# Optimization experiments

Hardware: AMD Instinct MI355X
Metric: run time of the kernel (lower is better)

Reference implementation:

```python
import jax, jax.numpy as jnp
import numpy as np

INPUT_DIM = 512
HIDDEN_DIM = 512
T, B = 512, 128


def setup_inputs() -> dict:
    key = jax.random.key(0)
    ks = jax.random.split(key, 9)
    s_in = 1.0 / np.sqrt(INPUT_DIM + HIDDEN_DIM)
    d = INPUT_DIM + HIDDEN_DIM
    inputs = jax.random.normal(ks[0], (T, B, INPUT_DIM), dtype=jnp.float32)
    def lin(kw, kb):
        W = jax.random.uniform(kw, (HIDDEN_DIM, d), minval=-s_in, maxval=s_in, dtype=jnp.float32)
        b = jax.random.uniform(kb, (HIDDEN_DIM,), minval=-s_in, maxval=s_in, dtype=jnp.float32)
        return W, b
    Wf, bf = lin(ks[1], ks[2])
    Wi, bi = lin(ks[3], ks[4])
    Wg, bg = lin(ks[5], ks[6])
    Wo, bo = lin(ks[7], ks[8])
    return {"inputs": inputs, "Wf": Wf, "bf": bf, "Wi": Wi, "bi": bi,
            "Wg": Wg, "bg": bg, "Wo": Wo, "bo": bo}


def _lstm(inputs, Wf, bf, Wi, bi, Wg, bg, Wo, bo):
    B_ = inputs.shape[1]
    h0 = jnp.zeros((B_, HIDDEN_DIM), dtype=inputs.dtype)
    c0 = jnp.zeros((B_, HIDDEN_DIM), dtype=inputs.dtype)

    def step(carry, x):
        hx, cx = carry
        combined = jnp.concatenate([x, hx], axis=1)  # [B, input+hidden]
        f = jax.nn.sigmoid(combined @ Wf.T + bf)
        i = jax.nn.sigmoid(combined @ Wi.T + bi)
        g = jnp.tanh(combined @ Wg.T + bg)
        o = jax.nn.sigmoid(combined @ Wo.T + bo)
        cx = f * cx + i * g
        hx = o * jnp.tanh(cx)
        return (hx, cx), hx

    (hx, cx), outputs = jax.lax.scan(step, (h0, c0), inputs)
    return outputs, (hx, cx)


def reference(inputs, Wf, bf, Wi, bi, Wg, bg, Wo, bo):
    return _lstm(inputs, Wf, bf, Wi, bi, Wg, bg, Wo, bo)
```

## Files before the change

kernel.cpp:

```cpp
#include <hip/hip_runtime.h>
#include <stdint.h>

#define T_STEPS 512
#define BATCH   128
#define HID     512
#define KTOT    1024

typedef __attribute__((ext_vector_type(8))) short          bf16x8;
typedef __attribute__((ext_vector_type(8))) unsigned short u16x8;
typedef __attribute__((ext_vector_type(4))) float          f32x4;

__device__ inline unsigned short f2bf(float f) {
    union { float f; unsigned u; } x; x.f = f;
    unsigned r = x.u + 0x7FFFu + ((x.u >> 16) & 1u);
    return (unsigned short)(r >> 16);
}

__device__ inline float sigmoidf_(float x) { return 1.f / (1.f + __expf(-x)); }
__device__ inline float tanhf_(float x)    { float e = __expf(2.f * x); return 1.f - 2.f / (e + 1.f); }

__global__ void cast_x_kernel(const float* __restrict__ x, unsigned short* __restrict__ y, int n) {
    int i = (blockIdx.x * blockDim.x + threadIdx.x) * 8;
    if (i >= n) return;
    float4 a = *(const float4*)(x + i);
    float4 b = *(const float4*)(x + i + 4);
    u16x8 v;
    v[0] = f2bf(a.x); v[1] = f2bf(a.y); v[2] = f2bf(a.z); v[3] = f2bf(a.w);
    v[4] = f2bf(b.x); v[5] = f2bf(b.y); v[6] = f2bf(b.z); v[7] = f2bf(b.w);
    *(u16x8*)(y + i) = v;
}

__device__ inline void load_x32(const float* xf, const unsigned short* xbf, int use_xbf,
                                size_t off, uint4& a, uint4& b) {
    if (use_xbf) {
        const uint4* p = (const uint4*)(xbf + off);
        a = p[0]; b = p[1];
    } else {
        const float4* p = (const float4*)(xf + off);
        float4 f0 = p[0], f1 = p[1], f2 = p[2], f3 = p[3];
        u16x8 v;
        v[0] = f2bf(f0.x); v[1] = f2bf(f0.y); v[2] = f2bf(f0.z); v[3] = f2bf(f0.w);
        v[4] = f2bf(f1.x); v[5] = f2bf(f1.y); v[6] = f2bf(f1.z); v[7] = f2bf(f1.w);
        a = *(uint4*)&v;
        u16x8 w;
        w[0] = f2bf(f2.x); w[1] = f2bf(f2.y); w[2] = f2bf(f2.z); w[3] = f2bf(f2.w);
        w[4] = f2bf(f3.x); w[5] = f2bf(f3.y); w[6] = f2bf(f3.z); w[7] = f2bf(f3.w);
        b = *(uint4*)&w;
    }
}

__global__ __launch_bounds__(512, 2) void lstm_kernel(
    const float* __restrict__ xf,
    const unsigned short* __restrict__ xbf,
    const float* __restrict__ Wf, const float* __restrict__ bfv,
    const float* __restrict__ Wi, const float* __restrict__ biv,
    const float* __restrict__ Wg, const float* __restrict__ bgv,
    const float* __restrict__ Wo, const float* __restrict__ bov,
    float* __restrict__ out,
    unsigned int* __restrict__ flags,
    unsigned short* __restrict__ hbuf,
    int use_xbf)
{
    __shared__ __align__(16) unsigned short comb[16][1048];
    __shared__ float gatesl[4][16][33];

    const int tid  = threadIdx.x;
    const int bgc  = blockIdx.x >> 4;
    const int cg   = blockIdx.x & 15;
    const int w    = tid >> 6;
    const int lane = tid & 63;
    const int gate = w & 3;
    const int uh   = w >> 2;
    const int n    = lane & 15;
    const int quad = lane >> 4;
    const int unit = cg * 32 + uh * 16 + n;

    const float* Wp = (gate == 0) ? Wf : (gate == 1) ? Wi : (gate == 2) ? Wg : Wo;
    const float* bp = (gate == 0) ? bfv : (gate == 1) ? biv : (gate == 2) ? bgv : bov;
    const float bias = bp[unit];

    bf16x8 wfr[32];
    const float* wrow = Wp + (size_t)unit * KTOT;
#pragma unroll
    for (int kk = 0; kk < 32; ++kk) {
        const float4* p = (const float4*)(wrow + kk * 32 + quad * 8);
        float4 a = p[0], b = p[1];
        u16x8 v;
        v[0] = f2bf(a.x); v[1] = f2bf(a.y); v[2] = f2bf(a.z); v[3] = f2bf(a.w);
        v[4] = f2bf(b.x); v[5] = f2bf(b.y); v[6] = f2bf(b.z); v[7] = f2bf(b.w);
        wfr[kk] = (bf16x8)v;
    }

    const int srow = tid >> 5;
    const int scol = tid & 31;

    const int bc = srow, uc = scol;
    float creg = 0.f;
    const int bglob = bgc * 16 + bc;
    const int uglob = cg * 32 + uc;

    const size_t xstride = (size_t)HID;

    {
        uint4 a, b;
        load_x32(xf, xbf, use_xbf, ((size_t)(0 * BATCH + bgc * 16 + srow)) * xstride + scol * 16, a, b);
        *(uint4*)&comb[srow][scol * 16]     = a;
        *(uint4*)&comb[srow][scol * 16 + 8] = b;
        uint4 z = {0u, 0u, 0u, 0u};
        *(uint4*)&comb[srow][512 + scol * 16]     = z;
        *(uint4*)&comb[srow][512 + scol * 16 + 8] = z;
    }
    __syncthreads();

    f32x4 axa = {0.f, 0.f, 0.f, 0.f}, axb = {0.f, 0.f, 0.f, 0.f};
#pragma unroll
    for (int kk = 0; kk < 16; kk += 2) {
        bf16x8 a0 = *(const bf16x8*)&comb[n][kk * 32 + quad * 8];
        bf16x8 a1 = *(const bf16x8*)&comb[n][(kk + 1) * 32 + quad * 8];
        axa = __builtin_amdgcn_mfma_f32_16x16x32_bf16(a0, wfr[kk],     axa, 0, 0, 0);
        axb = __builtin_amdgcn_mfma_f32_16x16x32_bf16(a1, wfr[kk + 1], axb, 0, 0, 0);
    }

    uint4 pfa, pfb;
    load_x32(xf, xbf, use_xbf, ((size_t)(1 * BATCH + bgc * 16 + srow)) * xstride + scol * 16, pfa, pfb);

    for (int t = 0; t < T_STEPS; ++t) {
        if (t > 0) {
            if (lane < 16) {
                unsigned int* fp = flags + ((size_t)(t - 1) * 8 + bgc) * 16 + lane;
                while (__hip_atomic_load(fp, __ATOMIC_RELAXED, __HIP_MEMORY_SCOPE_AGENT) == 0u) {}
            }
            const unsigned long long* src = (const unsigned long long*)
                (hbuf + (size_t)((t - 1) & 1) * BATCH * HID + (size_t)(bgc * 16 + srow) * HID + scol * 16);
            unsigned long long v0 = __hip_atomic_load(src + 0, __ATOMIC_RELAXED, __HIP_MEMORY_SCOPE_AGENT);
            unsigned long long v1 = __hip_atomic_load(src + 1, __ATOMIC_RELAXED, __HIP_MEMORY_SCOPE_AGENT);
            unsigned long long v2 = __hip_atomic_load(src + 2, __ATOMIC_RELAXED, __HIP_MEMORY_SCOPE_AGENT);
            unsigned long long v3 = __hip_atomic_load(src + 3, __ATOMIC_RELAXED, __HIP_MEMORY_SCOPE_AGENT);
            uint4 a, b;
            a.x = (unsigned)v0; a.y = (unsigned)(v0 >> 32);
            a.z = (unsigned)v1; a.w = (unsigned)(v1 >> 32);
            b.x = (unsigned)v2; b.y = (unsigned)(v2 >> 32);
            b.z = (unsigned)v3; b.w = (unsigned)(v3 >> 32);
            *(uint4*)&comb[srow][512 + scol * 16]     = a;
            *(uint4*)&comb[srow][512 + scol * 16 + 8] = b;
        }
        __syncthreads();

#pragma unroll
        for (int kk = 16; kk < 32; kk += 2) {
            bf16x8 a0 = *(const bf16x8*)&comb[n][kk * 32 + quad * 8];
            bf16x8 a1 = *(const bf16x8*)&comb[n][(kk + 1) * 32 + quad * 8];
            axa = __builtin_amdgcn_mfma_f32_16x16x32_bf16(a0, wfr[kk],     axa, 0, 0, 0);
            axb = __builtin_amdgcn_mfma_f32_16x16x32_bf16(a1, wfr[kk + 1], axb, 0, 0, 0);
        }

#pragma unroll
        for (int r = 0; r < 4; ++r) {
            float v = axa[r] + axb[r] + bias;
            v = (gate == 2) ? tanhf_(v) : sigmoidf_(v);
            gatesl[gate][quad * 4 + r][uh * 16 + n] = v;
        }
        if (t + 1 < T_STEPS) {
            *(uint4*)&comb[srow][scol * 16]     = pfa;
            *(uint4*)&comb[srow][scol * 16 + 8] = pfb;
        }
        __syncthreads();

        {
            float fv = gatesl[0][bc][uc], iv = gatesl[1][bc][uc];
            float gv = gatesl[2][bc][uc], ov = gatesl[3][bc][uc];
            float cn = fv * creg + iv * gv;
            creg = cn;
            float hv = ov * tanhf_(cn);
            unsigned int us  = (unsigned int)f2bf(hv);
            unsigned int us1 = (unsigned int)__shfl_down((int)us, 1);
            if ((uc & 1) == 0) {
                unsigned int pv = us | (us1 << 16);
                unsigned int* hp = (unsigned int*)(hbuf + (size_t)(t & 1) * BATCH * HID
                                                   + (size_t)bglob * HID + uglob);
                __hip_atomic_store(hp, pv, __ATOMIC_RELAXED, __HIP_MEMORY_SCOPE_AGENT);
            }
            out[(size_t)t * BATCH * HID + (size_t)bglob * HID + uglob] = hv;
            if (t == T_STEPS - 1) {
                out[(size_t)T_STEPS * BATCH * HID + (size_t)bglob * HID + uglob] = hv;
                out[(size_t)T_STEPS * BATCH * HID + BATCH * HID + (size_t)bglob * HID + uglob] = cn;
            }
        }

        if (t + 1 < T_STEPS) {
            axa = (f32x4){0.f, 0.f, 0.f, 0.f};
            axb = (f32x4){0.f, 0.f, 0.f, 0.f};
#pragma unroll
            for (int kk = 0; kk < 16; kk += 2) {
                bf16x8 a0 = *(const bf16x8*)&comb[n][kk * 32 + quad * 8];
                bf16x8 a1 = *(const bf16x8*)&comb[n][(kk + 1) * 32 + quad * 8];
                axa = __builtin_amdgcn_mfma_f32_16x16x32_bf16(a0, wfr[kk],     axa, 0, 0, 0);
                axb = __builtin_amdgcn_mfma_f32_16x16x32_bf16(a1, wfr[kk + 1], axb, 0, 0, 0);
            }
        }

        __builtin_amdgcn_s_waitcnt(0);
        __syncthreads();
        if (tid == 0) {
            __hip_atomic_store(flags + ((size_t)t * 8 + bgc) * 16 + cg, 1u,
                               __ATOMIC_RELAXED, __HIP_MEMORY_SCOPE_AGENT);
        }
        if (t + 2 < T_STEPS) {
            load_x32(xf, xbf, use_xbf,
                     ((size_t)((t + 2) * BATCH + bgc * 16 + srow)) * xstride + scol * 16, pfa, pfb);
        }
    }
}

extern "C" void kernel_launch(void* const* d_in, const int* in_sizes, int n_in,
                              void* d_out, int out_size, void* d_ws, size_t ws_size,
                              hipStream_t stream) {
    (void)in_sizes; (void)n_in; (void)out_size;
    const float* x   = (const float*)d_in[0];
    const float* Wf  = (const float*)d_in[1];
    const float* bfv = (const float*)d_in[2];
    const float* Wi  = (const float*)d_in[3];
    const float* biv = (const float*)d_in[4];
    const float* Wg  = (const float*)d_in[5];
    const float* bgv = (const float*)d_in[6];
    const float* Wo  = (const float*)d_in[7];
    const float* bov = (const float*)d_in[8];
    float* out = (float*)d_out;

    unsigned char* ws = (unsigned char*)d_ws;
    unsigned int*   flags = (unsigned int*)ws;
    unsigned short* hbuf  = (unsigned short*)(ws + 262144);
    unsigned short* xbf   = (unsigned short*)(ws + 524288);

    size_t need = 524288 + (size_t)T_STEPS * BATCH * HID * 2;
    int use_xbf = (ws_size >= need) ? 1 : 0;

    hipMemsetAsync(flags, 0, 262144, stream);
    if (use_xbf) {
        int nelem = T_STEPS * BATCH * HID;
        cast_x_kernel<<<nelem / (256 * 8), 256, 0, stream>>>(x, xbf, nelem);
    }
    lstm_kernel<<<dim3(128), dim3(512), 0, stream>>>(
        x, xbf, Wf, bfv, Wi, biv, Wg, bgv, Wo, bov, out, flags, hbuf, use_xbf);
}
```

Baseline: 1.940 ms.

## Replace per-step flag barrier with step-tagged h packets polled directly

Removes the separate flag array and the per-step waitcnt plus block barrier plus flag store. Each hidden-state word pair is now written as a 64-bit packet that carries the step number, so consumers poll the data itself until every tag matches. The next step's h is loaded speculatively at the end of each iteration to hide latency. The trade-off is that the h exchange traffic doubles and each thread spins on eight loads instead of a few lanes spinning on one flag.

New measurement: 2.226 ms. 1.15x slower.

```diff
diff --git a/kernel.cpp b/kernel.cpp
--- a/kernel.cpp
+++ b/kernel.cpp
@@ -5,6 +5,7 @@
 #define BATCH   128
 #define HID     512
 #define KTOT    1024
+#define HPAIRS  (BATCH * 256)
 
 typedef __attribute__((ext_vector_type(8))) short          bf16x8;
 typedef __attribute__((ext_vector_type(8))) unsigned short u16x8;
@@ -57,8 +58,7 @@
     const float* __restrict__ Wg, const float* __restrict__ bgv,
     const float* __restrict__ Wo, const float* __restrict__ bov,
     float* __restrict__ out,
-    unsigned int* __restrict__ flags,
-    unsigned short* __restrict__ hbuf,
+    unsigned long long* __restrict__ hbuf,
     int use_xbf)
 {
     __shared__ __align__(16) unsigned short comb[16][1048];
@@ -98,12 +98,13 @@
     float creg = 0.f;
     const int bglob = bgc * 16 + bc;
     const int uglob = cg * 32 + uc;
+    const int bgrow = bgc * 16 + srow;
 
     const size_t xstride = (size_t)HID;
 
     {
         uint4 a, b;
-        load_x32(xf, xbf, use_xbf, ((size_t)(0 * BATCH + bgc * 16 + srow)) * xstride + scol * 16, a, b);
+        load_x32(xf, xbf, use_xbf, ((size_t)(0 * BATCH + bgrow)) * xstride + scol * 16, a, b);
         *(uint4*)&comb[srow][scol * 16]     = a;
         *(uint4*)&comb[srow][scol * 16 + 8] = b;
         uint4 z = {0u, 0u, 0u, 0u};
@@ -122,25 +123,31 @@
     }
 
     uint4 pfa, pfb;
-    load_x32(xf, xbf, use_xbf, ((size_t)(1 * BATCH + bgc * 16 + srow)) * xstride + scol * 16, pfa, pfb);
+    load_x32(xf, xbf, use_xbf, ((size_t)(1 * BATCH + bgrow)) * xstride + scol * 16, pfa, pfb);
+
+    unsigned long long pv[8];
 
     for (int t = 0; t < T_STEPS; ++t) {
         if (t > 0) {
-            if (lane < 16) {
-                unsigned int* fp = flags + ((size_t)(t - 1) * 8 + bgc) * 16 + lane;
-                while (__hip_atomic_load(fp, __ATOMIC_RELAXED, __HIP_MEMORY_SCOPE_AGENT) == 0u) {}
-            }
-            const unsigned long long* src = (const unsigned long long*)
-                (hbuf + (size_t)((t - 1) & 1) * BATCH * HID + (size_t)(bgc * 16 + srow) * HID + scol * 16);
-            unsigned long long v0 = __hip_atomic_load(src + 0, __ATOMIC_RELAXED, __HIP_MEMORY_SCOPE_AGENT);
-            unsigned long long v1 = __hip_atomic_load(src + 1, __ATOMIC_RELAXED, __HIP_MEMORY_SCOPE_AGENT);
-            unsigned long long v2 = __hip_atomic_load(src + 2, __ATOMIC_RELAXED, __HIP_MEMORY_SCOPE_AGENT);
-            unsigned long long v3 = __hip_atomic_load(src + 3, __ATOMIC_RELAXED, __HIP_MEMORY_SCOPE_AGENT);
+            const unsigned long long* hs = hbuf + (size_t)((t - 1) & 1) * HPAIRS
+                                         + (size_t)bgrow * 256 + (size_t)scol * 8;
+            const unsigned int want = (unsigned int)t;
+            bool ok = true;
+#pragma unroll
+            for (int j = 0; j < 8; ++j) ok = ok && ((unsigned int)(pv[j] >> 32) == want);
+            while (!ok) {
+#pragma unroll
+                for (int j = 0; j < 8; ++j)
+                    pv[j] = __hip_atomic_load(hs + j, __ATOMIC_RELAXED, __HIP_MEMORY_SCOPE_AGENT);
+                ok = true;
+#pragma unroll
+                for (int j = 0; j < 8; ++j) ok = ok && ((unsigned int)(pv[j] >> 32) == want);
+            }
             uint4 a, b;
-            a.x = (unsigned)v0; a.y = (unsigned)(v0 >> 32);
-            a.z = (unsigned)v1; a.w = (unsigned)(v1 >> 32);
-            b.x = (unsigned)v2; b.y = (unsigned)(v2 >> 32);
-            b.z = (unsigned)v3; b.w = (unsigned)(v3 >> 32);
+            a.x = (unsigned int)pv[0]; a.y = (unsigned int)pv[1];
+            a.z = (unsigned int)pv[2]; a.w = (unsigned int)pv[3];
+            b.x = (unsigned int)pv[4]; b.y = (unsigned int)pv[5];
+            b.z = (unsigned int)pv[6]; b.w = (unsigned int)pv[7];
             *(uint4*)&comb[srow][512 + scol * 16]     = a;
             *(uint4*)&comb[srow][512 + scol * 16 + 8] = b;
         }
@@ -174,11 +181,12 @@
             float hv = ov * tanhf_(cn);
             unsigned int us  = (unsigned int)f2bf(hv);
             unsigned int us1 = (unsigned int)__shfl_down((int)us, 1);
-            if ((uc & 1) == 0) {
-                unsigned int pv = us | (us1 << 16);
-                unsigned int* hp = (unsigned int*)(hbuf + (size_t)(t & 1) * BATCH * HID
-                                                   + (size_t)bglob * HID + uglob);
-                __hip_atomic_store(hp, pv, __ATOMIC_RELAXED, __HIP_MEMORY_SCOPE_AGENT);
+            if (t + 1 < T_STEPS && (uc & 1) == 0) {
+                unsigned long long pkt = ((unsigned long long)(unsigned int)(t + 1) << 32)
+                                       | (unsigned long long)(us | (us1 << 16));
+                unsigned long long* hp = hbuf + (size_t)(t & 1) * HPAIRS
+                                       + (size_t)bglob * 256 + (size_t)(uglob >> 1);
+                __hip_atomic_store(hp, pkt, __ATOMIC_RELAXED, __HIP_MEMORY_SCOPE_AGENT);
             }
             out[(size_t)t * BATCH * HID + (size_t)bglob * HID + uglob] = hv;
             if (t == T_STEPS - 1) {
@@ -199,15 +207,16 @@
             }
         }
 
-        __builtin_amdgcn_s_waitcnt(0);
-        __syncthreads();
-        if (tid == 0) {
-            __hip_atomic_store(flags + ((size_t)t * 8 + bgc) * 16 + cg, 1u,
-                               __ATOMIC_RELAXED, __HIP_MEMORY_SCOPE_AGENT);
-        }
         if (t + 2 < T_STEPS) {
             load_x32(xf, xbf, use_xbf,
-                     ((size_t)((t + 2) * BATCH + bgc * 16 + srow)) * xstride + scol * 16, pfa, pfb);
+                     ((size_t)((t + 2) * BATCH + bgrow)) * xstride + scol * 16, pfa, pfb);
+        }
+        if (t + 1 < T_STEPS) {
+            const unsigned long long* hs2 = hbuf + (size_t)(t & 1) * HPAIRS
+                                          + (size_t)bgrow * 256 + (size_t)scol * 8;
+#pragma unroll
+            for (int j = 0; j < 8; ++j)
+                pv[j] = __hip_atomic_load(hs2 + j, __ATOMIC_RELAXED, __HIP_MEMORY_SCOPE_AGENT);
         }
     }
 }
@@ -228,18 +237,17 @@
     float* out = (float*)d_out;
 
     unsigned char* ws = (unsigned char*)d_ws;
-    unsigned int*   flags = (unsigned int*)ws;
-    unsigned short* hbuf  = (unsigned short*)(ws + 262144);
-    unsigned short* xbf   = (unsigned short*)(ws + 524288);
+    unsigned long long* hbuf = (unsigned long long*)ws;
+    unsigned short*     xbf  = (unsigned short*)(ws + 524288);
 
     size_t need = 524288 + (size_t)T_STEPS * BATCH * HID * 2;
     int use_xbf = (ws_size >= need) ? 1 : 0;
 
-    hipMemsetAsync(flags, 0, 262144, stream);
+    hipMemsetAsync(hbuf, 0, 524288, stream);
     if (use_xbf) {
         int nelem = T_STEPS * BATCH * HID;
         cast_x_kernel<<<nelem / (256 * 8), 256, 0, stream>>>(x, xbf, nelem);
     }
     lstm_kernel<<<dim3(128), dim3(512), 0, stream>>>(
-        x, xbf, Wf, bfv, Wi, biv, Wg, bgv, Wo, bov, out, flags, hbuf, use_xbf);
-}
+        x, xbf, Wf, bfv, Wi, biv, Wg, bgv, Wo, bov, out, hbuf, use_xbf);
+}
```

## Replace per-block flags and barrier with per-wave atomic counter signaling

Applied to the files above, without the earlier changes.

Drops the __syncthreads before the cross-block flag store: every wave now increments one shared counter per batch group and step, and waiting waves spin on a single counter until it reaches 128 (16 blocks x 8 waves) instead of polling 16 separate flags. The output stores are moved after the signal so global writes of h no longer delay the handoff, and the last step skips the unneeded hbuf write and signal. This is meant to cut barrier and flag-polling latency on the serial critical path. The cost is contended atomic adds on one address, and correctness now relies on each wave's own waitcnt ordering its hbuf stores before its increment.

After: 3.036 ms. 1.57x slower.

```diff
diff --git a/kernel.cpp b/kernel.cpp
--- a/kernel.cpp
+++ b/kernel.cpp
@@ -57,7 +57,7 @@
     const float* __restrict__ Wg, const float* __restrict__ bgv,
     const float* __restrict__ Wo, const float* __restrict__ bov,
     float* __restrict__ out,
-    unsigned int* __restrict__ flags,
+    unsigned int* __restrict__ ctr,
     unsigned short* __restrict__ hbuf,
     int use_xbf)
 {
@@ -98,12 +98,13 @@
     float creg = 0.f;
     const int bglob = bgc * 16 + bc;
     const int uglob = cg * 32 + uc;
+    const int bgrow = bgc * 16 + srow;
 
     const size_t xstride = (size_t)HID;
 
     {
         uint4 a, b;
-        load_x32(xf, xbf, use_xbf, ((size_t)(0 * BATCH + bgc * 16 + srow)) * xstride + scol * 16, a, b);
+        load_x32(xf, xbf, use_xbf, ((size_t)(0 * BATCH + bgrow)) * xstride + scol * 16, a, b);
         *(uint4*)&comb[srow][scol * 16]     = a;
         *(uint4*)&comb[srow][scol * 16 + 8] = b;
         uint4 z = {0u, 0u, 0u, 0u};
@@ -122,16 +123,16 @@
     }
 
     uint4 pfa, pfb;
-    load_x32(xf, xbf, use_xbf, ((size_t)(1 * BATCH + bgc * 16 + srow)) * xstride + scol * 16, pfa, pfb);
+    load_x32(xf, xbf, use_xbf, ((size_t)(1 * BATCH + bgrow)) * xstride + scol * 16, pfa, pfb);
 
     for (int t = 0; t < T_STEPS; ++t) {
         if (t > 0) {
-            if (lane < 16) {
-                unsigned int* fp = flags + ((size_t)(t - 1) * 8 + bgc) * 16 + lane;
-                while (__hip_atomic_load(fp, __ATOMIC_RELAXED, __HIP_MEMORY_SCOPE_AGENT) == 0u) {}
+            if (lane == 0) {
+                const unsigned int* cp = ctr + ((size_t)(t - 1) * 8 + bgc) * 16;
+                while (__hip_atomic_load(cp, __ATOMIC_RELAXED, __HIP_MEMORY_SCOPE_AGENT) < 128u) {}
             }
             const unsigned long long* src = (const unsigned long long*)
-                (hbuf + (size_t)((t - 1) & 1) * BATCH * HID + (size_t)(bgc * 16 + srow) * HID + scol * 16);
+                (hbuf + (size_t)((t - 1) & 1) * BATCH * HID + (size_t)bgrow * HID + scol * 16);
             unsigned long long v0 = __hip_atomic_load(src + 0, __ATOMIC_RELAXED, __HIP_MEMORY_SCOPE_AGENT);
             unsigned long long v1 = __hip_atomic_load(src + 1, __ATOMIC_RELAXED, __HIP_MEMORY_SCOPE_AGENT);
             unsigned long long v2 = __hip_atomic_load(src + 2, __ATOMIC_RELAXED, __HIP_MEMORY_SCOPE_AGENT);
@@ -166,24 +167,20 @@
         }
         __syncthreads();
 
+        float hv, cn;
         {
             float fv = gatesl[0][bc][uc], iv = gatesl[1][bc][uc];
             float gv = gatesl[2][bc][uc], ov = gatesl[3][bc][uc];
-            float cn = fv * creg + iv * gv;
+            cn = fv * creg + iv * gv;
             creg = cn;
-            float hv = ov * tanhf_(cn);
+            hv = ov * tanhf_(cn);
             unsigned int us  = (unsigned int)f2bf(hv);
             unsigned int us1 = (unsigned int)__shfl_down((int)us, 1);
-            if ((uc & 1) == 0) {
+            if (t + 1 < T_STEPS && (uc & 1) == 0) {
                 unsigned int pv = us | (us1 << 16);
                 unsigned int* hp = (unsigned int*)(hbuf + (size_t)(t & 1) * BATCH * HID
                                                    + (size_t)bglob * HID + uglob);
                 __hip_atomic_store(hp, pv, __ATOMIC_RELAXED, __HIP_MEMORY_SCOPE_AGENT);
-            }
-            out[(size_t)t * BATCH * HID + (size_t)bglob * HID + uglob] = hv;
-            if (t == T_STEPS - 1) {
-                out[(size_t)T_STEPS * BATCH * HID + (size_t)bglob * HID + uglob] = hv;
-                out[(size_t)T_STEPS * BATCH * HID + BATCH * HID + (size_t)bglob * HID + uglob] = cn;
             }
         }
 
@@ -200,14 +197,19 @@
         }
 
         __builtin_amdgcn_s_waitcnt(0);
-        __syncthreads();
-        if (tid == 0) {
-            __hip_atomic_store(flags + ((size_t)t * 8 + bgc) * 16 + cg, 1u,
-                               __ATOMIC_RELAXED, __HIP_MEMORY_SCOPE_AGENT);
+        if (lane == 0 && t + 1 < T_STEPS) {
+            __hip_atomic_fetch_add(ctr + ((size_t)t * 8 + bgc) * 16, 1u,
+                                   __ATOMIC_RELAXED, __HIP_MEMORY_SCOPE_AGENT);
+        }
+
+        out[(size_t)t * BATCH * HID + (size_t)bglob * HID + uglob] = hv;
+        if (t == T_STEPS - 1) {
+            out[(size_t)T_STEPS * BATCH * HID + (size_t)bglob * HID + uglob] = hv;
+            out[(size_t)T_STEPS * BATCH * HID + BATCH * HID + (size_t)bglob * HID + uglob] = cn;
         }
         if (t + 2 < T_STEPS) {
             load_x32(xf, xbf, use_xbf,
-                     ((size_t)((t + 2) * BATCH + bgc * 16 + srow)) * xstride + scol * 16, pfa, pfb);
+                     ((size_t)((t + 2) * BATCH + bgrow)) * xstride + scol * 16, pfa, pfb);
         }
     }
 }
@@ -228,18 +230,18 @@
     float* out = (float*)d_out;
 
     unsigned char* ws = (unsigned char*)d_ws;
-    unsigned int*   flags = (unsigned int*)ws;
-    unsigned short* hbuf  = (unsigned short*)(ws + 262144);
-    unsigned short* xbf   = (unsigned short*)(ws + 524288);
+    unsigned int*   ctr  = (unsigned int*)ws;
+    unsigned short* hbuf = (unsigned short*)(ws + 262144);
+    unsigned short* xbf  = (unsigned short*)(ws + 524288);
 
     size_t need = 524288 + (size_t)T_STEPS * BATCH * HID * 2;
     int use_xbf = (ws_size >= need) ? 1 : 0;
 
-    hipMemsetAsync(flags, 0, 262144, stream);
+    hipMemsetAsync(ctr, 0, 262144, stream);
     if (use_xbf) {
         int nelem = T_STEPS * BATCH * HID;
         cast_x_kernel<<<nelem / (256 * 8), 256, 0, stream>>>(x, xbf, nelem);
     }
     lstm_kernel<<<dim3(128), dim3(512), 0, stream>>>(
-        x, xbf, Wf, bfv, Wi, biv, Wg, bgv, Wo, bov, out, flags, hbuf, use_xbf);
-}
+        x, xbf, Wf, bfv, Wi, biv, Wg, bgv, Wo, bov, out, ctr, hbuf, use_xbf);
+}
```

## Split K across waves and compute all four gates per wave with LDS reduction

Applied to the files above, without the earlier changes.

Each wave used to own one gate and walk the full K=1024 dimension in a serial chain of MFMAs. Now each wave owns a quarter of K and computes all four gates, giving four independent accumulator chains, and the partial sums are reduced through shared memory in the elementwise stage. The aim is a shorter dependent MFMA chain per step on the recurrent critical path and more MFMA-level parallelism. The cost is extra LDS traffic and storage for the partials, plus a 4-way reduction per output element.

After: 1.899 ms. 2.1% less time.

```diff
diff --git a/kernel.cpp b/kernel.cpp
--- a/kernel.cpp
+++ b/kernel.cpp
@@ -62,33 +62,36 @@
     int use_xbf)
 {
     __shared__ __align__(16) unsigned short comb[16][1048];
-    __shared__ float gatesl[4][16][33];
+    __shared__ float gp[4][4][16][34];
 
     const int tid  = threadIdx.x;
     const int bgc  = blockIdx.x >> 4;
     const int cg   = blockIdx.x & 15;
     const int w    = tid >> 6;
     const int lane = tid & 63;
-    const int gate = w & 3;
+    const int kh   = w & 3;
     const int uh   = w >> 2;
     const int n    = lane & 15;
     const int quad = lane >> 4;
     const int unit = cg * 32 + uh * 16 + n;
 
-    const float* Wp = (gate == 0) ? Wf : (gate == 1) ? Wi : (gate == 2) ? Wg : Wo;
-    const float* bp = (gate == 0) ? bfv : (gate == 1) ? biv : (gate == 2) ? bgv : bov;
-    const float bias = bp[unit];
-
-    bf16x8 wfr[32];
-    const float* wrow = Wp + (size_t)unit * KTOT;
-#pragma unroll
-    for (int kk = 0; kk < 32; ++kk) {
-        const float4* p = (const float4*)(wrow + kk * 32 + quad * 8);
-        float4 a = p[0], b = p[1];
-        u16x8 v;
-        v[0] = f2bf(a.x); v[1] = f2bf(a.y); v[2] = f2bf(a.z); v[3] = f2bf(a.w);
-        v[4] = f2bf(b.x); v[5] = f2bf(b.y); v[6] = f2bf(b.z); v[7] = f2bf(b.w);
-        wfr[kk] = (bf16x8)v;
+    bf16x8 wfr[4][8];
+    {
+        const float* Wptr[4] = {Wf, Wi, Wg, Wo};
+#pragma unroll
+        for (int g = 0; g < 4; ++g) {
+            const float* wrow = Wptr[g] + (size_t)unit * KTOT;
+#pragma unroll
+            for (int j = 0; j < 8; ++j) {
+                const int kk = (j < 4) ? (kh * 4 + j) : (16 + kh * 4 + (j - 4));
+                const float4* p = (const float4*)(wrow + kk * 32 + quad * 8);
+                float4 a = p[0], b = p[1];
+                u16x8 v;
+                v[0] = f2bf(a.x); v[1] = f2bf(a.y); v[2] = f2bf(a.z); v[3] = f2bf(a.w);
+                v[4] = f2bf(b.x); v[5] = f2bf(b.y); v[6] = f2bf(b.z); v[7] = f2bf(b.w);
+                wfr[g][j] = (bf16x8)v;
+            }
+        }
     }
 
     const int srow = tid >> 5;
@@ -98,12 +101,17 @@
     float creg = 0.f;
     const int bglob = bgc * 16 + bc;
     const int uglob = cg * 32 + uc;
+    const int bgrow = bgc * 16 + srow;
+
+    float biasv[4];
+    biasv[0] = bfv[uglob]; biasv[1] = biv[uglob];
+    biasv[2] = bgv[uglob]; biasv[3] = bov[uglob];
 
     const size_t xstride = (size_t)HID;
 
     {
         uint4 a, b;
-        load_x32(xf, xbf, use_xbf, ((size_t)(0 * BATCH + bgc * 16 + srow)) * xstride + scol * 16, a, b);
+        load_x32(xf, xbf, use_xbf, ((size_t)(0 * BATCH + bgrow)) * xstride + scol * 16, a, b);
         *(uint4*)&comb[srow][scol * 16]     = a;
         *(uint4*)&comb[srow][scol * 16 + 8] = b;
         uint4 z = {0u, 0u, 0u, 0u};
@@ -112,17 +120,23 @@
     }
     __syncthreads();
 
-    f32x4 axa = {0.f, 0.f, 0.f, 0.f}, axb = {0.f, 0.f, 0.f, 0.f};
-#pragma unroll
-    for (int kk = 0; kk < 16; kk += 2) {
-        bf16x8 a0 = *(const bf16x8*)&comb[n][kk * 32 + quad * 8];
-        bf16x8 a1 = *(const bf16x8*)&comb[n][(kk + 1) * 32 + quad * 8];
-        axa = __builtin_amdgcn_mfma_f32_16x16x32_bf16(a0, wfr[kk],     axa, 0, 0, 0);
-        axb = __builtin_amdgcn_mfma_f32_16x16x32_bf16(a1, wfr[kk + 1], axb, 0, 0, 0);
+    f32x4 acc[4];
+#pragma unroll
+    for (int g = 0; g < 4; ++g) acc[g] = (f32x4){0.f, 0.f, 0.f, 0.f};
+    {
+        bf16x8 af[4];
+#pragma unroll
+        for (int j = 0; j < 4; ++j)
+            af[j] = *(const bf16x8*)&comb[n][(kh * 4 + j) * 32 + quad * 8];
+#pragma unroll
+        for (int j = 0; j < 4; ++j)
+#pragma unroll
+            for (int g = 0; g < 4; ++g)
+                acc[g] = __builtin_amdgcn_mfma_f32_16x16x32_bf16(af[j], wfr[g][j], acc[g], 0, 0, 0);
     }
 
     uint4 pfa, pfb;
-    load_x32(xf, xbf, use_xbf, ((size_t)(1 * BATCH + bgc * 16 + srow)) * xstride + scol * 16, pfa, pfb);
+    load_x32(xf, xbf, use_xbf, ((size_t)(1 * BATCH + bgrow)) * xstride + scol * 16, pfa, pfb);
 
     for (int t = 0; t < T_STEPS; ++t) {
         if (t > 0) {
@@ -131,7 +145,7 @@
                 while (__hip_atomic_load(fp, __ATOMIC_RELAXED, __HIP_MEMORY_SCOPE_AGENT) == 0u) {}
             }
             const unsigned long long* src = (const unsigned long long*)
-                (hbuf + (size_t)((t - 1) & 1) * BATCH * HID + (size_t)(bgc * 16 + srow) * HID + scol * 16);
+                (hbuf + (size_t)((t - 1) & 1) * BATCH * HID + (size_t)bgrow * HID + scol * 16);
             unsigned long long v0 = __hip_atomic_load(src + 0, __ATOMIC_RELAXED, __HIP_MEMORY_SCOPE_AGENT);
             unsigned long long v1 = __hip_atomic_load(src + 1, __ATOMIC_RELAXED, __HIP_MEMORY_SCOPE_AGENT);
             unsigned long long v2 = __hip_atomic_load(src + 2, __ATOMIC_RELAXED, __HIP_MEMORY_SCOPE_AGENT);
@@ -146,20 +160,23 @@
         }
         __syncthreads();
 
-#pragma unroll
-        for (int kk = 16; kk < 32; kk += 2) {
-            bf16x8 a0 = *(const bf16x8*)&comb[n][kk * 32 + quad * 8];
-            bf16x8 a1 = *(const bf16x8*)&comb[n][(kk + 1) * 32 + quad * 8];
-            axa = __builtin_amdgcn_mfma_f32_16x16x32_bf16(a0, wfr[kk],     axa, 0, 0, 0);
-            axb = __builtin_amdgcn_mfma_f32_16x16x32_bf16(a1, wfr[kk + 1], axb, 0, 0, 0);
-        }
-
-#pragma unroll
-        for (int r = 0; r < 4; ++r) {
-            float v = axa[r] + axb[r] + bias;
-            v = (gate == 2) ? tanhf_(v) : sigmoidf_(v);
-            gatesl[gate][quad * 4 + r][uh * 16 + n] = v;
-        }
+        {
+            bf16x8 af[4];
+#pragma unroll
+            for (int j = 0; j < 4; ++j)
+                af[j] = *(const bf16x8*)&comb[n][(16 + kh * 4 + j) * 32 + quad * 8];
+#pragma unroll
+            for (int j = 0; j < 4; ++j)
+#pragma unroll
+                for (int g = 0; g < 4; ++g)
+                    acc[g] = __builtin_amdgcn_mfma_f32_16x16x32_bf16(af[j], wfr[g][4 + j], acc[g], 0, 0, 0);
+        }
+
+#pragma unroll
+        for (int g = 0; g < 4; ++g)
+#pragma unroll
+            for (int r = 0; r < 4; ++r)
+                gp[kh][g][quad * 4 + r][uh * 16 + n] = acc[g][r];
         if (t + 1 < T_STEPS) {
             *(uint4*)&comb[srow][scol * 16]     = pfa;
             *(uint4*)&comb[srow][scol * 16 + 8] = pfb;
@@ -167,8 +184,14 @@
         __syncthreads();
 
         {
-            float fv = gatesl[0][bc][uc], iv = gatesl[1][bc][uc];
-            float gv = gatesl[2][bc][uc], ov = gatesl[3][bc][uc];
+            float s0 = gp[0][0][bc][uc] + gp[1][0][bc][uc] + gp[2][0][bc][uc] + gp[3][0][bc][uc] + biasv[0];
+            float s1 = gp[0][1][bc][uc] + gp[1][1][bc][uc] + gp[2][1][bc][uc] + gp[3][1][bc][uc] + biasv[1];
+            float s2 = gp[0][2][bc][uc] + gp[1][2][bc][uc] + gp[2][2][bc][uc] + gp[3][2][bc][uc] + biasv[2];
+            float s3 = gp[0][3][bc][uc] + gp[1][3][bc][uc] + gp[2][3][bc][uc] + gp[3][3][bc][uc] + biasv[3];
+            float fv = sigmoidf_(s0);
+            float iv = sigmoidf_(s1);
+            float gv = tanhf_(s2);
+            float ov = sigmoidf_(s3);
             float cn = fv * creg + iv * gv;
             creg = cn;
             float hv = ov * tanhf_(cn);
@@ -188,15 +211,17 @@
         }
 
         if (t + 1 < T_STEPS) {
-            axa = (f32x4){0.f, 0.f, 0.f, 0.f};
-            axb = (f32x4){0.f, 0.f, 0.f, 0.f};
-#pragma unroll
-            for (int kk = 0; kk < 16; kk += 2) {
-                bf16x8 a0 = *(const bf16x8*)&comb[n][kk * 32 + quad * 8];
-                bf16x8 a1 = *(const bf16x8*)&comb[n][(kk + 1) * 32 + quad * 8];
-                axa = __builtin_amdgcn_mfma_f32_16x16x32_bf16(a0, wfr[kk],     axa, 0, 0, 0);
-                axb = __builtin_amdgcn_mfma_f32_16x16x32_bf16(a1, wfr[kk + 1], axb, 0, 0, 0);
-            }
+#pragma unroll
+            for (int g = 0; g < 4; ++g) acc[g] = (f32x4){0.f, 0.f, 0.f, 0.f};
+            bf16x8 af[4];
+#pragma unroll
+            for (int j = 0; j < 4; ++j)
+                af[j] = *(const bf16x8*)&comb[n][(kh * 4 + j) * 32 + quad * 8];
+#pragma unroll
+            for (int j = 0; j < 4; ++j)
+#pragma unroll
+                for (int g = 0; g < 4; ++g)
+                    acc[g] = __builtin_amdgcn_mfma_f32_16x16x32_bf16(af[j], wfr[g][j], acc[g], 0, 0, 0);
         }
 
         __builtin_amdgcn_s_waitcnt(0);
@@ -207,7 +232,7 @@
         }
         if (t + 2 < T_STEPS) {
             load_x32(xf, xbf, use_xbf,
-                     ((size_t)((t + 2) * BATCH + bgc * 16 + srow)) * xstride + scol * 16, pfa, pfb);
+                     ((size_t)((t + 2) * BATCH + bgrow)) * xstride + scol * 16, pfa, pfb);
         }
     }
 }
```
